# Performance work log

Measured on AMD Instinct MI355X. Metric: run time of the kernel, lower is better.

The kernel has to match this reference:

```python
import jax, jax.numpy as jnp
import numpy as np

B, S, D, H = 4, 2048, 512, 8
DH = D // H  # depth per head = 64


def setup_inputs() -> dict:
    key = jax.random.key(0)
    ks = jax.random.split(key, 8)
    scale = 1.0 / np.sqrt(D)
    return {
        "query": jax.random.normal(ks[0], (B, S, D), jnp.float32),
        "key": jax.random.normal(ks[1], (B, S, D), jnp.float32),
        "value": jax.random.normal(ks[2], (B, S, D), jnp.float32),
        "mask": jax.random.randint(ks[3], (B, S), 0, 2, jnp.int32),
        "wq_w": jax.random.normal(ks[4], (D, D), jnp.float32) * scale,
        "wq_b": jnp.zeros((D,), jnp.float32),
        "wk_w": jax.random.normal(ks[5], (D, D), jnp.float32) * scale,
        "wk_b": jnp.zeros((D,), jnp.float32),
        "wv_w": jax.random.normal(ks[6], (D, D), jnp.float32) * scale,
        "wv_b": jnp.zeros((D,), jnp.float32),
        "wo_w": jax.random.normal(ks[7], (D, D), jnp.float32) * scale,
        "wo_b": jnp.zeros((D,), jnp.float32),
    }


def _split_heads(x):
    # [B, S, D] -> [B, H, S, DH]
    b, s, _ = x.shape
    return x.reshape(b, s, H, DH).transpose(0, 2, 1, 3)


def reference(query, key, value, mask, wq_w, wq_b, wk_w, wk_b, wv_w, wv_b, wo_w, wo_b):
    q = _split_heads(query @ wq_w + wq_b)   # [B,H,S,DH]
    k = _split_heads(key @ wk_w + wk_b)
    v = _split_heads(value @ wv_w + wv_b)

    scale = 1.0 / jnp.sqrt(jnp.asarray(DH, jnp.float32))
    logits = jnp.einsum('bhqd,bhkd->bhqk', q, k) * scale  # [B,H,S,S]
    # additive key-padding mask: 1 -> masked (adds -1e9)
    m = mask.astype(logits.dtype)[:, None, None, :]  # [B,1,1,S]
    logits = logits + m * -1e9
    weights = jax.nn.softmax(logits, axis=-1)
    attn = jnp.einsum('bhqk,bhkd->bhqd', weights, v)  # [B,H,S,DH]
    attn = attn.transpose(0, 2, 1, 3).reshape(query.shape[0], -1, D)  # [B,S,D]
    return attn @ wo_w + wo_b
```

## Files before the change

### kernel.cpp

```cpp
#include <hip/hip_runtime.h>
#include <stdint.h>

#define QSCALE (0.125f * 1.44269504088896340736f)
#define MASKNEG (-1.442695e9f)

typedef unsigned short u16;
typedef unsigned int u32;
typedef __bf16 bf16x8 __attribute__((ext_vector_type(8)));
typedef float f32x4 __attribute__((ext_vector_type(4)));
typedef float f32x16 __attribute__((ext_vector_type(16)));
typedef u16 u16x8 __attribute__((ext_vector_type(8)));
typedef u32 u32x4 __attribute__((ext_vector_type(4)));

__device__ __forceinline__ u16 f2bf(float f) {
  u32 u = __float_as_uint(f);
  u += 0x7fffu + ((u >> 16) & 1u);
  return (u16)(u >> 16);
}

__device__ __forceinline__ u32 cvtpk(float lo, float hi) {
  u32 d;
  asm("v_cvt_pk_bf16_f32 %0, %1, %2" : "=v"(d) : "v"(lo), "v"(hi));
  return d;
}

__device__ __forceinline__ void plswap(u32& a, u32& b) {
  asm("v_permlane32_swap_b32 %0, %1" : "+v"(a), "+v"(b));
}

__device__ __forceinline__ void gload16(const void* src, void* ldsbase) {
  __builtin_amdgcn_global_load_lds(
      (const __attribute__((address_space(1))) u32*)src,
      (__attribute__((address_space(3))) u32*)ldsbase, 16, 0, 0);
}

__global__ __launch_bounds__(256) void conv_w(const float* __restrict__ wq,
                                              const float* __restrict__ wk,
                                              const float* __restrict__ wv,
                                              const float* __restrict__ wo,
                                              u16* __restrict__ wT) {
  const float* src = (blockIdx.z == 0) ? wq : (blockIdx.z == 1) ? wk
                    : (blockIdx.z == 2) ? wv : wo;
  u16* dst = wT + (size_t)blockIdx.z * 262144;
  __shared__ float t[64][65];
  const int n0 = blockIdx.x * 64, k0 = blockIdx.y * 64;
  const int lr = threadIdx.x >> 6, lc = threadIdx.x & 63;
#pragma unroll
  for (int it = 0; it < 16; ++it) {
    const int row = it * 4 + lr;
    t[row][lc] = src[(size_t)(k0 + row) * 512 + n0 + lc];
  }
  __syncthreads();
#pragma unroll
  for (int it = 0; it < 16; ++it) {
    const int row = it * 4 + lr;
    dst[(size_t)(n0 + row) * 512 + k0 + lc] = f2bf(t[lc][row]);
  }
}

__global__ __launch_bounds__(256, 3) void gemm_qkv(
    const float* __restrict__ xqf, const float* __restrict__ xkf,
    const float* __restrict__ xvf, const u16* __restrict__ wT,
    const float* __restrict__ bq, const float* __restrict__ bk,
    const float* __restrict__ bv, u16* __restrict__ qws, u16* __restrict__ kws,
    u16* __restrict__ vTw) {
  __shared__ __align__(16) char lds[49152];
  const int hw = blockIdx.x;
  const int lg = (hw & 7) * 96 + (hw >> 3);
  const int z = lg >> 8;
  const int rem = lg & 255;
  const int m0 = (rem >> 2) * 128, n0 = (rem & 3) * 128;
  const float* A = (z == 0) ? xqf : (z == 1) ? xkf : xvf;
  const u16* Bt = wT + (size_t)z * 262144;
  const float* bias = (z == 0) ? bq : (z == 1) ? bk : bv;

  const int tid = threadIdx.x;
  const int lane = tid & 63;
  const int wave = tid >> 6;
  const int wm = wave >> 1, wn = wave & 1;
  const int h4 = lane >> 4, l15 = lane & 15;

  f32x4 acc[4][4] = {};

  auto stage = [&](int buf, int kt) {
    const int k0 = kt * 32;
    char* baseA = lds + buf * 24576;
    char* baseB = baseA + 16384;
    {
      const int sxA = tid & 7;
#pragma unroll
      for (int c = 0; c < 4; ++c) {
        const int row = c * 32 + (tid >> 3);
        const int sx = sxA ^ (row & 7);
        gload16(A + (size_t)(m0 + row) * 512 + k0 + sx * 4,
                baseA + row * 128 + (sx << 4));
      }
    }
    {
      const int sxB = tid & 3;
#pragma unroll
      for (int c = 0; c < 2; ++c) {
        const int row = c * 64 + (tid >> 2);
        const int sx = sxB ^ (row & 3);
        gload16(Bt + (size_t)(n0 + row) * 512 + k0 + sx * 8,
                baseB + row * 64 + (sx << 4));
      }
    }
  };

  auto compute = [&](int buf) {
    const char* bA = lds + buf * 24576;
    const char* bB = bA + 16384;
    bf16x8 av[4], bv[4];
#pragma unroll
    for (int i = 0; i < 4; ++i) {
      const int row = wm * 64 + i * 16 + l15;
      const f32x4 lo =
          *(const f32x4*)(bA + row * 128 + (((h4 * 2) ^ (row & 7)) << 4));
      const f32x4 hi =
          *(const f32x4*)(bA + row * 128 + (((h4 * 2 + 1) ^ (row & 7)) << 4));
      u32x4 w;
      w[0] = cvtpk(lo[0], lo[1]);
      w[1] = cvtpk(lo[2], lo[3]);
      w[2] = cvtpk(hi[0], hi[1]);
      w[3] = cvtpk(hi[2], hi[3]);
      av[i] = __builtin_bit_cast(bf16x8, w);
    }
#pragma unroll
    for (int j = 0; j < 4; ++j) {
      const int row = wn * 64 + j * 16 + l15;
      bv[j] = *(const bf16x8*)(bB + row * 64 + ((h4 ^ (row & 3)) << 4));
    }
#pragma unroll
    for (int i = 0; i < 4; ++i)
#pragma unroll
      for (int j = 0; j < 4; ++j)
        acc[i][j] = __builtin_amdgcn_mfma_f32_16x16x32_bf16(av[i], bv[j],
                                                            acc[i][j], 0, 0, 0);
  };

  stage(0, 0);
  __syncthreads();
#pragma unroll
  for (int kt = 0; kt < 16; ++kt) {
    const int cur = kt & 1;
    if (kt < 15) stage(cur ^ 1, kt + 1);
    compute(cur);
    __syncthreads();
  }

#pragma unroll
  for (int j = 0; j < 4; ++j) {
    const int n = n0 + wn * 64 + j * 16 + l15;
    const float bn = bias[n];
    const int h = n >> 6, dh = n & 63;
#pragma unroll
    for (int i = 0; i < 4; ++i) {
#pragma unroll
      for (int r = 0; r < 4; ++r) {
        const int rg = m0 + wm * 64 + i * 16 + h4 * 4 + r;
        const int b = rg >> 11, s = rg & 2047;
        const int bh = b * 8 + h;
        const float val = acc[i][j][r] + bn;
        if (z == 0) {
          qws[((size_t)bh * 2048 + s) * 64 + dh] = f2bf(val * QSCALE);
        } else if (z == 1) {
          kws[((size_t)bh * 2048 + s) * 64 + dh] = f2bf(val);
        } else {
          vTw[((size_t)bh * 64 + dh) * 2048 + s] = f2bf(val);
        }
      }
    }
  }
}

__global__ __launch_bounds__(512, 4) void attn_fwd(
    const u16* __restrict__ qws, const u16* __restrict__ kws,
    const u16* __restrict__ vTw, const int* __restrict__ mask,
    u16* __restrict__ attn) {
  __shared__ __align__(16) char ldsK[32768];
  __shared__ __align__(16) char ldsV[32768];
  __shared__ __align__(16) float biasLDS[2048];
  __shared__ float lShA[128];

  const int bh = blockIdx.x;
  const int qt = blockIdx.y;
  const int b = bh >> 3;
  const int tid = threadIdx.x;
  const int lane = tid & 63, wave = tid >> 6;
  const int half = wave >> 2, wl = wave & 3;
  const int l31 = lane & 31, h5 = lane >> 5;

  {
    const int4 m4 = *(const int4*)(mask + b * 2048 + tid * 4);
    float4 bv;
    bv.x = m4.x ? MASKNEG : 0.0f;
    bv.y = m4.y ? MASKNEG : 0.0f;
    bv.z = m4.z ? MASKNEG : 0.0f;
    bv.w = m4.w ? MASKNEG : 0.0f;
    *(float4*)(biasLDS + tid * 4) = bv;
  }
  asm volatile("s_waitcnt lgkmcnt(0)" ::: "memory");

  const u16* qrow_p = qws + ((size_t)bh * 2048 + qt * 128 + wl * 32 + l31) * 64;
  bf16x8 qb[4];
#pragma unroll
  for (int c = 0; c < 4; ++c)
    qb[c] = *(const bf16x8*)(qrow_p + c * 16 + h5 * 8);

  const int rowb = l31 * 128;
  int kxs[4];
#pragma unroll
  for (int c = 0; c < 4; ++c) kxs[c] = ((2 * c + h5) ^ (l31 & 7)) << 4;

  char* myK = ldsK + half * 16384;
  char* myV = ldsV + half * 16384;
  const int srow = wl * 8 + (lane >> 3);
  const int sc16 = lane & 7;

  auto stage = [&](int buf, int ktg) {
#pragma unroll
    for (int c = 0; c < 2; ++c) {
      const int row = c * 32 + srow;
      const int xc = (sc16 ^ (row & 7)) << 3;
      gload16(kws + ((size_t)bh * 2048 + ktg * 64 + row) * 64 + xc,
              myK + buf * 8192 + c * 4096 + (wl << 10));
      gload16(vTw + ((size_t)bh * 64 + row) * 2048 + ktg * 64 + xc,
              myV + buf * 8192 + c * 4096 + (wl << 10));
    }
  };

  f32x16 o0 = {}, o1 = {};
  float rsp0 = 0.f, rsp1 = 0.f, rsp2 = 0.f, rsp3 = 0.f;

  auto do_subtile = [&](const char* kb, const char* vb, const float* biasT,
                        int stByte, int c0) {
    f32x16 sv;
#pragma unroll
    for (int g = 0; g < 4; ++g) {
      const f32x4 bq4 = *(const f32x4*)(biasT + g * 8 + h5 * 4);
      sv[g * 4 + 0] = bq4[0];
      sv[g * 4 + 1] = bq4[1];
      sv[g * 4 + 2] = bq4[2];
      sv[g * 4 + 3] = bq4[3];
    }
    __builtin_amdgcn_s_setprio(1);
#pragma unroll
    for (int c = 0; c < 4; ++c) {
      const bf16x8 kf = *(const bf16x8*)(kb + stByte + rowb + kxs[c]);
      sv = __builtin_amdgcn_mfma_f32_32x32x16_bf16(kf, qb[c], sv, 0, 0, 0);
    }
    __builtin_amdgcn_s_setprio(0);
    float p[16];
#pragma unroll
    for (int i = 0; i < 16; ++i) p[i] = __builtin_amdgcn_exp2f(sv[i]);
    rsp0 += p[0] + p[4] + p[8] + p[12];
    rsp1 += p[1] + p[5] + p[9] + p[13];
    rsp2 += p[2] + p[6] + p[10] + p[14];
    rsp3 += p[3] + p[7] + p[11] + p[15];
    u32 paw[2][4];
#pragma unroll
    for (int lc = 0; lc < 2; ++lc) {
      u32 a1 = cvtpk(p[lc * 8 + 0], p[lc * 8 + 1]);
      u32 b1 = cvtpk(p[lc * 8 + 4], p[lc * 8 + 5]);
      u32 a2 = cvtpk(p[lc * 8 + 2], p[lc * 8 + 3]);
      u32 b2 = cvtpk(p[lc * 8 + 6], p[lc * 8 + 7]);
      plswap(a1, b1);
      plswap(a2, b2);
      paw[lc][0] = a1; paw[lc][1] = a2; paw[lc][2] = b1; paw[lc][3] = b2;
    }
    __builtin_amdgcn_s_setprio(1);
#pragma unroll
    for (int lc = 0; lc < 2; ++lc) {
      u32x4 w = {paw[lc][0], paw[lc][1], paw[lc][2], paw[lc][3]};
      const bf16x8 pa = __builtin_bit_cast(bf16x8, w);
      const bf16x8 vf0 = *(const bf16x8*)(vb + rowb + kxs[c0 + lc]);
      o0 = __builtin_amdgcn_mfma_f32_32x32x16_bf16(pa, vf0, o0, 0, 0, 0);
      const bf16x8 vf1 = *(const bf16x8*)(vb + 4096 + rowb + kxs[c0 + lc]);
      o1 = __builtin_amdgcn_mfma_f32_32x32x16_bf16(pa, vf1, o1, 0, 0, 0);
    }
    __builtin_amdgcn_s_setprio(0);
  };

  stage(0, half * 16);

  for (int kt = 0; kt < 16; ++kt) {
    const int cur = kt & 1;
    const int ktg = half * 16 + kt;
    if (kt < 15) {
      stage(cur ^ 1, ktg + 1);
      asm volatile("s_waitcnt vmcnt(4)" ::: "memory");
    } else {
      asm volatile("s_waitcnt vmcnt(0)" ::: "memory");
    }
    __builtin_amdgcn_sched_barrier(0);
    __builtin_amdgcn_s_barrier();
    const char* kb = myK + cur * 8192;
    const char* vb = myV + cur * 8192;
    const float* biasT = biasLDS + ktg * 64;
    do_subtile(kb, vb, biasT, 0, 0);
    do_subtile(kb, vb, biasT + 32, 4096, 2);
    __builtin_amdgcn_sched_barrier(0);
    __builtin_amdgcn_s_barrier();
  }

  float rs = (rsp0 + rsp1) + (rsp2 + rsp3);
  rs += __shfl_xor(rs, 32);

  float* oSh2 = (float*)ldsK;
  u16* trb = (u16*)ldsV;
  if (half == 1) {
#pragma unroll
    for (int reg = 0; reg < 16; ++reg) {
      oSh2[(wl * 32 + reg) * 64 + lane] = o0[reg];
      oSh2[(wl * 32 + 16 + reg) * 64 + lane] = o1[reg];
    }
    if (h5 == 0) lShA[wl * 32 + l31] = rs;
  }
  __syncthreads();
  if (half == 0) {
    const float ltot = rs + lShA[wl * 32 + l31];
    const float linv = 1.0f / ltot;
#pragma unroll
    for (int reg = 0; reg < 16; ++reg) {
      const int q = (reg & 3) + 8 * (reg >> 2) + 4 * h5;
      const float inv = __shfl(linv, q);
      const float v0 = (o0[reg] + oSh2[(wl * 32 + reg) * 64 + lane]) * inv;
      const float v1 = (o1[reg] + oSh2[(wl * 32 + 16 + reg) * 64 + lane]) * inv;
      trb[(wl * 32 + q) * 64 + l31] = f2bf(v0);
      trb[(wl * 32 + q) * 64 + 32 + l31] = f2bf(v1);
    }
  }
  __syncthreads();
  const int h = bh & 7;
#pragma unroll
  for (int i = 0; i < 2; ++i) {
    const int ii = tid + i * 512;
    const int row = ii >> 3;
    const int c8 = (ii & 7) * 8;
    const u16x8 vv = *(const u16x8*)(trb + row * 64 + c8);
    const int grow = b * 2048 + qt * 128 + row;
    *(u16x8*)(attn + (size_t)grow * 512 + h * 64 + c8) = vv;
  }
}

__global__ __launch_bounds__(256, 3) void gemm_out(const u16* __restrict__ attn,
                                                   const u16* __restrict__ woT,
                                                   const float* __restrict__ bo,
                                                   float* __restrict__ out) {
  __shared__ __align__(16) char lds[49152];
  const int hw = blockIdx.x;
  const int lg = (hw & 7) * 64 + (hw >> 3);
  const int m0 = (lg >> 2) * 64, n0 = (lg & 3) * 128;

  const int tid = threadIdx.x;
  const int lane = tid & 63;
  const int wave = tid >> 6;
  const int wm = wave >> 1, wn = wave & 1;
  const int srow = tid >> 3;
  const int sc16 = tid & 7;

  f32x4 acc[2][4] = {};

  auto stage = [&](int buf, int kt) {
    const int k0 = kt * 64;
    char* base = lds + buf * 24576;
#pragma unroll
    for (int c = 0; c < 2; ++c) {
      const int row = c * 32 + srow;
      const int xc = (sc16 ^ (row & 7)) << 3;
      gload16(attn + (size_t)(m0 + row) * 512 + k0 + xc,
              base + c * 4096 + (wave << 10));
    }
#pragma unroll
    for (int c = 0; c < 4; ++c) {
      const int row = c * 32 + srow;
      const int xc = (sc16 ^ (row & 7)) << 3;
      gload16(woT + (size_t)(n0 + row) * 512 + k0 + xc,
              base + 8192 + c * 4096 + (wave << 10));
    }
  };

  auto compute = [&](int buf) {
    const char* bA = lds + buf * 24576;
    const char* bB = bA + 8192;
#pragma unroll
    for (int kk = 0; kk < 2; ++kk) {
      const int c16 = kk * 4 + (lane >> 4);
      bf16x8 av[2], bv[4];
#pragma unroll
      for (int i = 0; i < 2; ++i) {
        const int row = wm * 32 + i * 16 + (lane & 15);
        av[i] = *(const bf16x8*)(bA + row * 128 + ((c16 ^ (row & 7)) << 4));
      }
#pragma unroll
      for (int j = 0; j < 4; ++j) {
        const int row = wn * 64 + j * 16 + (lane & 15);
        bv[j] = *(const bf16x8*)(bB + row * 128 + ((c16 ^ (row & 7)) << 4));
      }
#pragma unroll
      for (int i = 0; i < 2; ++i)
#pragma unroll
        for (int j = 0; j < 4; ++j)
          acc[i][j] = __builtin_amdgcn_mfma_f32_16x16x32_bf16(av[i], bv[j],
                                                              acc[i][j], 0, 0, 0);
    }
  };

  stage(0, 0);
  __syncthreads();
#pragma unroll
  for (int kt = 0; kt < 8; ++kt) {
    const int cur = kt & 1;
    if (kt < 7) stage(cur ^ 1, kt + 1);
    compute(cur);
    __syncthreads();
  }

#pragma unroll
  for (int j = 0; j < 4; ++j) {
    const int n = n0 + wn * 64 + j * 16 + (lane & 15);
    const float bn = bo[n];
#pragma unroll
    for (int i = 0; i < 2; ++i) {
      const int rbase = m0 + wm * 32 + i * 16 + ((lane >> 4) << 2);
#pragma unroll
      for (int r = 0; r < 4; ++r)
        out[(size_t)(rbase + r) * 512 + n] = acc[i][j][r] + bn;
    }
  }
}

extern "C" void kernel_launch(void* const* d_in, const int* in_sizes, int n_in,
                              void* d_out, int out_size, void* d_ws,
                              size_t ws_size, hipStream_t stream) {
  (void)in_sizes; (void)n_in; (void)out_size; (void)ws_size;
  const float* q = (const float*)d_in[0];
  const float* k = (const float*)d_in[1];
  const float* v = (const float*)d_in[2];
  const int* mask = (const int*)d_in[3];
  const float* wq = (const float*)d_in[4];
  const float* bq = (const float*)d_in[5];
  const float* wk = (const float*)d_in[6];
  const float* bk = (const float*)d_in[7];
  const float* wv = (const float*)d_in[8];
  const float* bv = (const float*)d_in[9];
  const float* wo = (const float*)d_in[10];
  const float* bo = (const float*)d_in[11];

  u16* attnb = (u16*)d_ws;
  u16* wT = attnb + 4194304;
  u16* qws = wT + 1048576;
  u16* kws = qws + 4194304;
  u16* vTw = kws + 4194304;
  float* out = (float*)d_out;

  conv_w<<<dim3(8, 8, 4), 256, 0, stream>>>(wq, wk, wv, wo, wT);
  gemm_qkv<<<768, 256, 0, stream>>>(q, k, v, wT, bq, bk, bv, qws, kws, vTw);
  attn_fwd<<<dim3(32, 16), 512, 0, stream>>>(qws, kws, vTw, mask, attnb);
  gemm_out<<<512, 256, 0, stream>>>(attnb, wT + 786432, bo, out);
}
```

Measured before the change: 100.7 us.

## Replace LDS-staged GEMMs with direct global-to-register MFMA loads

Both projection GEMMs (QKV and output) drop LDS double-buffering and load MFMA operand fragments straight from global memory into registers. Each wave now computes its own 32x64 tile, with the QKV grid doubled to 1536 blocks of 128x64 tiles. This removes the LDS staging and barrier overhead and relaxes the occupancy limit from the launch bounds. The cost is that operands are no longer shared through LDS, so each wave re-reads the same weight rows from global memory and the kernels lean on L1/L2 for reuse. The loads are also strided per lane, which may coalesce poorly.

```diff
diff --git a/kernel.cpp b/kernel.cpp
--- a/kernel.cpp
+++ b/kernel.cpp
@@ -32,6 +32,15 @@
   __builtin_amdgcn_global_load_lds(
       (const __attribute__((address_space(1))) u32*)src,
       (__attribute__((address_space(3))) u32*)ldsbase, 16, 0, 0);
+}
+
+__device__ __forceinline__ bf16x8 cvt8(const f32x4& lo, const f32x4& hi) {
+  u32x4 w;
+  w[0] = cvtpk(lo[0], lo[1]);
+  w[1] = cvtpk(lo[2], lo[3]);
+  w[2] = cvtpk(hi[0], hi[1]);
+  w[3] = cvtpk(hi[2], hi[3]);
+  return __builtin_bit_cast(bf16x8, w);
 }
 
 __global__ __launch_bounds__(256) void conv_w(const float* __restrict__ wq,
@@ -58,107 +67,62 @@
   }
 }
 
-__global__ __launch_bounds__(256, 3) void gemm_qkv(
+__global__ __launch_bounds__(256) void gemm_qkv(
     const float* __restrict__ xqf, const float* __restrict__ xkf,
     const float* __restrict__ xvf, const u16* __restrict__ wT,
     const float* __restrict__ bq, const float* __restrict__ bk,
     const float* __restrict__ bv, u16* __restrict__ qws, u16* __restrict__ kws,
     u16* __restrict__ vTw) {
-  __shared__ __align__(16) char lds[49152];
   const int hw = blockIdx.x;
-  const int lg = (hw & 7) * 96 + (hw >> 3);
-  const int z = lg >> 8;
-  const int rem = lg & 255;
-  const int m0 = (rem >> 2) * 128, n0 = (rem & 3) * 128;
+  const int lg = (hw & 7) * 192 + (hw >> 3);
+  const int z = lg >> 9;
+  const int rem = lg & 511;
+  const int m0 = (rem >> 3) * 128, n0 = (rem & 7) * 64;
   const float* A = (z == 0) ? xqf : (z == 1) ? xkf : xvf;
   const u16* Bt = wT + (size_t)z * 262144;
   const float* bias = (z == 0) ? bq : (z == 1) ? bk : bv;
 
   const int tid = threadIdx.x;
-  const int lane = tid & 63;
-  const int wave = tid >> 6;
-  const int wm = wave >> 1, wn = wave & 1;
+  const int lane = tid & 63, wave = tid >> 6;
   const int h4 = lane >> 4, l15 = lane & 15;
 
-  f32x4 acc[4][4] = {};
-
-  auto stage = [&](int buf, int kt) {
+  const float* a0 = A + (size_t)(m0 + wave * 32 + l15) * 512 + h4 * 8;
+  const float* a1 = a0 + 16 * 512;
+  const u16* bp = Bt + (size_t)(n0 + l15) * 512 + h4 * 8;
+
+  f32x4 acc[2][4] = {};
+#pragma unroll 4
+  for (int kt = 0; kt < 16; ++kt) {
     const int k0 = kt * 32;
-    char* baseA = lds + buf * 24576;
-    char* baseB = baseA + 16384;
-    {
-      const int sxA = tid & 7;
-#pragma unroll
-      for (int c = 0; c < 4; ++c) {
-        const int row = c * 32 + (tid >> 3);
-        const int sx = sxA ^ (row & 7);
-        gload16(A + (size_t)(m0 + row) * 512 + k0 + sx * 4,
-                baseA + row * 128 + (sx << 4));
-      }
-    }
-    {
-      const int sxB = tid & 3;
-#pragma unroll
-      for (int c = 0; c < 2; ++c) {
-        const int row = c * 64 + (tid >> 2);
-        const int sx = sxB ^ (row & 3);
-        gload16(Bt + (size_t)(n0 + row) * 512 + k0 + sx * 8,
-                baseB + row * 64 + (sx << 4));
-      }
-    }
-  };
-
-  auto compute = [&](int buf) {
-    const char* bA = lds + buf * 24576;
-    const char* bB = bA + 16384;
-    bf16x8 av[4], bv[4];
-#pragma unroll
-    for (int i = 0; i < 4; ++i) {
-      const int row = wm * 64 + i * 16 + l15;
-      const f32x4 lo =
-          *(const f32x4*)(bA + row * 128 + (((h4 * 2) ^ (row & 7)) << 4));
-      const f32x4 hi =
-          *(const f32x4*)(bA + row * 128 + (((h4 * 2 + 1) ^ (row & 7)) << 4));
-      u32x4 w;
-      w[0] = cvtpk(lo[0], lo[1]);
-      w[1] = cvtpk(lo[2], lo[3]);
-      w[2] = cvtpk(hi[0], hi[1]);
-      w[3] = cvtpk(hi[2], hi[3]);
-      av[i] = __builtin_bit_cast(bf16x8, w);
-    }
+    const f32x4 x0 = *(const f32x4*)(a0 + k0);
+    const f32x4 x1 = *(const f32x4*)(a0 + k0 + 4);
+    const f32x4 y0 = *(const f32x4*)(a1 + k0);
+    const f32x4 y1 = *(const f32x4*)(a1 + k0 + 4);
+    bf16x8 bv4[4];
+#pragma unroll
+    for (int j = 0; j < 4; ++j)
+      bv4[j] = *(const bf16x8*)(bp + (size_t)j * 16 * 512 + k0);
+    const bf16x8 av0 = cvt8(x0, x1);
+    const bf16x8 av1 = cvt8(y0, y1);
 #pragma unroll
     for (int j = 0; j < 4; ++j) {
-      const int row = wn * 64 + j * 16 + l15;
-      bv[j] = *(const bf16x8*)(bB + row * 64 + ((h4 ^ (row & 3)) << 4));
-    }
-#pragma unroll
-    for (int i = 0; i < 4; ++i)
-#pragma unroll
-      for (int j = 0; j < 4; ++j)
-        acc[i][j] = __builtin_amdgcn_mfma_f32_16x16x32_bf16(av[i], bv[j],
-                                                            acc[i][j], 0, 0, 0);
-  };
-
-  stage(0, 0);
-  __syncthreads();
-#pragma unroll
-  for (int kt = 0; kt < 16; ++kt) {
-    const int cur = kt & 1;
-    if (kt < 15) stage(cur ^ 1, kt + 1);
-    compute(cur);
-    __syncthreads();
+      acc[0][j] = __builtin_amdgcn_mfma_f32_16x16x32_bf16(av0, bv4[j],
+                                                          acc[0][j], 0, 0, 0);
+      acc[1][j] = __builtin_amdgcn_mfma_f32_16x16x32_bf16(av1, bv4[j],
+                                                          acc[1][j], 0, 0, 0);
+    }
   }
 
 #pragma unroll
   for (int j = 0; j < 4; ++j) {
-    const int n = n0 + wn * 64 + j * 16 + l15;
+    const int n = n0 + j * 16 + l15;
     const float bn = bias[n];
     const int h = n >> 6, dh = n & 63;
 #pragma unroll
-    for (int i = 0; i < 4; ++i) {
+    for (int i = 0; i < 2; ++i) {
 #pragma unroll
       for (int r = 0; r < 4; ++r) {
-        const int rg = m0 + wm * 64 + i * 16 + h4 * 4 + r;
+        const int rg = m0 + wave * 32 + i * 16 + h4 * 4 + r;
         const int b = rg >> 11, s = rg & 2047;
         const int bh = b * 8 + h;
         const float val = acc[i][j][r] + bn;
@@ -344,86 +308,48 @@
   }
 }
 
-__global__ __launch_bounds__(256, 3) void gemm_out(const u16* __restrict__ attn,
-                                                   const u16* __restrict__ woT,
-                                                   const float* __restrict__ bo,
-                                                   float* __restrict__ out) {
-  __shared__ __align__(16) char lds[49152];
+__global__ __launch_bounds__(256) void gemm_out(const u16* __restrict__ attn,
+                                                const u16* __restrict__ woT,
+                                                const float* __restrict__ bo,
+                                                float* __restrict__ out) {
   const int hw = blockIdx.x;
   const int lg = (hw & 7) * 64 + (hw >> 3);
-  const int m0 = (lg >> 2) * 64, n0 = (lg & 3) * 128;
+  const int m0 = (lg >> 3) * 128, n0 = (lg & 7) * 64;
 
   const int tid = threadIdx.x;
-  const int lane = tid & 63;
-  const int wave = tid >> 6;
-  const int wm = wave >> 1, wn = wave & 1;
-  const int srow = tid >> 3;
-  const int sc16 = tid & 7;
+  const int lane = tid & 63, wave = tid >> 6;
+  const int h4 = lane >> 4, l15 = lane & 15;
+
+  const u16* a0 = attn + (size_t)(m0 + wave * 32 + l15) * 512 + h4 * 8;
+  const u16* a1 = a0 + 16 * 512;
+  const u16* bp = woT + (size_t)(n0 + l15) * 512 + h4 * 8;
 
   f32x4 acc[2][4] = {};
-
-  auto stage = [&](int buf, int kt) {
-    const int k0 = kt * 64;
-    char* base = lds + buf * 24576;
-#pragma unroll
-    for (int c = 0; c < 2; ++c) {
-      const int row = c * 32 + srow;
-      const int xc = (sc16 ^ (row & 7)) << 3;
-      gload16(attn + (size_t)(m0 + row) * 512 + k0 + xc,
-              base + c * 4096 + (wave << 10));
-    }
-#pragma unroll
-    for (int c = 0; c < 4; ++c) {
-      const int row = c * 32 + srow;
-      const int xc = (sc16 ^ (row & 7)) << 3;
-      gload16(woT + (size_t)(n0 + row) * 512 + k0 + xc,
-              base + 8192 + c * 4096 + (wave << 10));
-    }
-  };
-
-  auto compute = [&](int buf) {
-    const char* bA = lds + buf * 24576;
-    const char* bB = bA + 8192;
-#pragma unroll
-    for (int kk = 0; kk < 2; ++kk) {
-      const int c16 = kk * 4 + (lane >> 4);
-      bf16x8 av[2], bv[4];
-#pragma unroll
-      for (int i = 0; i < 2; ++i) {
-        const int row = wm * 32 + i * 16 + (lane & 15);
-        av[i] = *(const bf16x8*)(bA + row * 128 + ((c16 ^ (row & 7)) << 4));
-      }
-#pragma unroll
-      for (int j = 0; j < 4; ++j) {
-        const int row = wn * 64 + j * 16 + (lane & 15);
-        bv[j] = *(const bf16x8*)(bB + row * 128 + ((c16 ^ (row & 7)) << 4));
-      }
-#pragma unroll
-      for (int i = 0; i < 2; ++i)
-#pragma unroll
-        for (int j = 0; j < 4; ++j)
-          acc[i][j] = __builtin_amdgcn_mfma_f32_16x16x32_bf16(av[i], bv[j],
-                                                              acc[i][j], 0, 0, 0);
-    }
-  };
-
-  stage(0, 0);
-  __syncthreads();
-#pragma unroll
-  for (int kt = 0; kt < 8; ++kt) {
-    const int cur = kt & 1;
-    if (kt < 7) stage(cur ^ 1, kt + 1);
-    compute(cur);
-    __syncthreads();
+#pragma unroll 4
+  for (int kt = 0; kt < 16; ++kt) {
+    const int k0 = kt * 32;
+    const bf16x8 av0 = *(const bf16x8*)(a0 + k0);
+    const bf16x8 av1 = *(const bf16x8*)(a1 + k0);
+    bf16x8 bv4[4];
+#pragma unroll
+    for (int j = 0; j < 4; ++j)
+      bv4[j] = *(const bf16x8*)(bp + (size_t)j * 16 * 512 + k0);
+#pragma unroll
+    for (int j = 0; j < 4; ++j) {
+      acc[0][j] = __builtin_amdgcn_mfma_f32_16x16x32_bf16(av0, bv4[j],
+                                                          acc[0][j], 0, 0, 0);
+      acc[1][j] = __builtin_amdgcn_mfma_f32_16x16x32_bf16(av1, bv4[j],
+                                                          acc[1][j], 0, 0, 0);
+    }
   }
 
 #pragma unroll
   for (int j = 0; j < 4; ++j) {
-    const int n = n0 + wn * 64 + j * 16 + (lane & 15);
+    const int n = n0 + j * 16 + l15;
     const float bn = bo[n];
 #pragma unroll
     for (int i = 0; i < 2; ++i) {
-      const int rbase = m0 + wm * 32 + i * 16 + ((lane >> 4) << 2);
+      const int rbase = m0 + wave * 32 + i * 16 + h4 * 4;
 #pragma unroll
       for (int r = 0; r < 4; ++r)
         out[(size_t)(rbase + r) * 512 + n] = acc[i][j][r] + bn;
@@ -456,7 +382,7 @@
   float* out = (float*)d_out;
 
   conv_w<<<dim3(8, 8, 4), 256, 0, stream>>>(wq, wk, wv, wo, wT);
-  gemm_qkv<<<768, 256, 0, stream>>>(q, k, v, wT, bq, bk, bv, qws, kws, vTw);
+  gemm_qkv<<<1536, 256, 0, stream>>>(q, k, v, wT, bq, bk, bv, qws, kws, vTw);
   attn_fwd<<<dim3(32, 16), 512, 0, stream>>>(qws, kws, vTw, mask, attnb);
   gemm_out<<<512, 256, 0, stream>>>(attnb, wT + 786432, bo, out);
 }
```

After: 174.2 us. 73.0% more time.
